# Optimization experiments

Hardware: AMD Instinct MI355X
Metric: run time of the kernel (lower is better)

The kernel has to match this reference:

```python
import jax, jax.numpy as jnp
import numpy as np

RESOLUTION = 2048
NUM_BEAMS = 256
K0 = 50.0
TWO_PI = 2.0 * np.pi


def setup_inputs() -> dict:
    key = jax.random.key(0)
    ks = jax.random.split(key, 6)
    # meshgrid buffers (indexing='ij')
    x = jnp.linspace(-1.0, 1.0, RESOLUTION, dtype=jnp.float32)
    y = jnp.linspace(-1.0, 1.0, RESOLUTION, dtype=jnp.float32)
    X, Y = jnp.meshgrid(x, y, indexing='ij')
    return {
        'theta': jax.random.uniform(ks[0], (NUM_BEAMS,), jnp.float32) * TWO_PI,
        'real': jax.random.normal(ks[1], (NUM_BEAMS,), jnp.float32) * 0.1,
        'imag': jax.random.normal(ks[2], (NUM_BEAMS,), jnp.float32) * 0.1,
        'x0': jax.random.uniform(ks[3], (NUM_BEAMS,), jnp.float32) * 2.0 - 1.0,
        'y0': jax.random.uniform(ks[4], (NUM_BEAMS,), jnp.float32) * 2.0 - 1.0,
        'log_sigma': jnp.zeros((NUM_BEAMS,), jnp.float32),
        'X': X,
        'Y': Y,
    }


def reference(theta, real, imag, x0, y0, log_sigma, X, Y):
    # Accumulate E = sum_i coeff_i * exp(i*phase_i) * envelope_i over beams,
    # carrying (E_re, E_im) through a scan so only grid-sized buffers live at once.
    def body(carry, p):
        E_re, E_im = carry
        th, re, im, px, py, ls = p
        kx = K0 * jnp.cos(th)
        ky = K0 * jnp.sin(th)
        sigma = jnp.exp(ls) + 0.001
        env = jnp.exp(-((X - px) ** 2 + (Y - py) ** 2) / sigma ** 2)
        phase = kx * X + ky * Y
        c = jnp.cos(phase)
        s = jnp.sin(phase)
        # (re + i*im) * (c + i*s) * env
        E_re = E_re + env * (re * c - im * s)
        E_im = E_im + env * (re * s + im * c)
        return (E_re, E_im), None

    params = jnp.stack([theta, real, imag, x0, y0, log_sigma], axis=1)  # [B, 6]
    zero = jnp.zeros_like(X)
    (E_re, E_im), _ = jax.lax.scan(body, (zero, zero), params)
    return E_re ** 2 + E_im ** 2  # |E|^2
```

## Files before the change

### kernel.cpp

```cpp
#include <hip/hip_runtime.h>
#include <math.h>

#define RES 2048
#define NB  256
#define PLANE (RES * NB)
#define STEP (2.0f / 2047.0f)

typedef _Float16 f16;
typedef _Float16 f16x8 __attribute__((ext_vector_type(8)));
typedef float    f32x16 __attribute__((ext_vector_type(16)));

__device__ __forceinline__ f16x8 neg8(f16x8 v) {
    union { f16x8 h; unsigned int u[4]; } x;
    x.h = v;
    #pragma unroll
    for (int i = 0; i < 4; ++i) x.u[i] ^= 0x80008000u;
    return x.h;
}


__global__ __launch_bounds__(256) void tables_frag(
    const float* __restrict__ theta, const float* __restrict__ reA,
    const float* __restrict__ imA, const float* __restrict__ x0A,
    const float* __restrict__ y0A, const float* __restrict__ lsA,
    f16* __restrict__ ws)
{
    f16* aRe = ws;
    f16* aIm = ws + PLANE;
    f16* bRe = ws + 2 * PLANE;
    f16* bIm = ws + 3 * PLANE;

    const int gid = blockIdx.x * 256 + threadIdx.x;
    const int l   = gid & 63;
    const int w   = gid >> 6;
    const int grow = (w >> 4) * 32 + (l & 31);
    const int b0   = (w & 15) * 16 + (l >> 5) * 8;
    const int e    = w * 512 + (l >> 5) * 256 + (l & 31) * 8;

    const float xv = -1.0f + (float)grow * STEP;

    float aRv[8], aIv[8], bRv[8], bIv[8];
    #pragma unroll
    for (int j = 0; j < 8; ++j) {
        const int b = b0 + j;
        const float th  = theta[b];
        const float sth = __sinf(th), cth = __cosf(th);
        const float kx = 50.0f * cth, ky = 50.0f * sth;
        const float sig = __expf(lsA[b]) + 0.001f;
        const float is2 = 1.0f / (sig * sig);
        const float re = reA[b], im = imA[b];

        const float phx = kx * xv;
        const float snx = __sinf(phx), csx = __cosf(phx);
        const float dx = xv - x0A[b];
        const float ex = __expf(-dx * dx * is2);
        aRv[j] = ex * (re * csx - im * snx);
        aIv[j] = ex * (re * snx + im * csx);

        const float phy = ky * xv;
        const float sny = __sinf(phy), csy = __cosf(phy);
        const float dy = xv - y0A[b];
        const float ey = __expf(-dy * dy * is2);
        bRv[j] = ey * csy;
        bIv[j] = ey * sny;
    }

    union { f16 h[8]; float4 v; } p;
    #pragma unroll
    for (int j = 0; j < 8; ++j) p.h[j] = (f16)aRv[j];
    *(float4*)&aRe[e] = p.v;
    #pragma unroll
    for (int j = 0; j < 8; ++j) p.h[j] = (f16)aIv[j];
    *(float4*)&aIm[e] = p.v;
    #pragma unroll
    for (int j = 0; j < 8; ++j) p.h[j] = (f16)bRv[j];
    *(float4*)&bRe[e] = p.v;
    #pragma unroll
    for (int j = 0; j < 8; ++j) p.h[j] = (f16)bIv[j];
    *(float4*)&bIm[e] = p.v;
}

__global__ __launch_bounds__(512) void gemm_frag(
    const f16* __restrict__ ws, float* __restrict__ out)
{
    const f16* aRe = ws;
    const f16* aIm = ws + PLANE;
    const f16* bRe = ws + 2 * PLANE;
    const f16* bIm = ws + 3 * PLANE;

    const int t    = threadIdx.x;
    const int lane = t & 63;
    const int wave = t >> 6;
    const int wm   = wave >> 2;
    const int wn   = wave & 3;
    const int la   = lane & 31;
    const int lg   = lane >> 5;

    const int flat = blockIdx.x;
    const int swz  = (flat & 7) * 32 + (flat >> 3);
    const int m0   = (swz >> 4) * 128;
    const int n0   = (swz & 15) * 128;

    const int laneOff = lg * 256 + la * 8;
    const int cA0 = ((m0 >> 5) + wm * 2 + 0) * 16;
    const int cA1 = ((m0 >> 5) + wm * 2 + 1) * 16;
    const int cB  = ((n0 >> 5) + wn) * 16;

    const f16* pAR0 = aRe + cA0 * 512 + laneOff;
    const f16* pAR1 = aRe + cA1 * 512 + laneOff;
    const f16* pAI0 = aIm + cA0 * 512 + laneOff;
    const f16* pAI1 = aIm + cA1 * 512 + laneOff;
    const f16* pBR  = bRe + cB  * 512 + laneOff;
    const f16* pBI  = bIm + cB  * 512 + laneOff;

    f32x16 accRe0 = (f32x16)0.0f, accIm0 = (f32x16)0.0f;
    f32x16 accRe1 = (f32x16)0.0f, accIm1 = (f32x16)0.0f;

    f16x8 aR0 = *(const f16x8*)pAR0;
    f16x8 aR1 = *(const f16x8*)pAR1;
    f16x8 aI0 = *(const f16x8*)pAI0;
    f16x8 aI1 = *(const f16x8*)pAI1;
    f16x8 bR  = *(const f16x8*)pBR;
    f16x8 bI  = *(const f16x8*)pBI;

    for (int kt = 0; kt < 16; ++kt) {
        const int nx = ((kt + 1) & 15) * 512;
        const f16x8 nR0 = *(const f16x8*)(pAR0 + nx);
        const f16x8 nR1 = *(const f16x8*)(pAR1 + nx);
        const f16x8 nI0 = *(const f16x8*)(pAI0 + nx);
        const f16x8 nI1 = *(const f16x8*)(pAI1 + nx);
        const f16x8 nBR = *(const f16x8*)(pBR  + nx);
        const f16x8 nBI = *(const f16x8*)(pBI  + nx);

        const f16x8 bN = neg8(bI);
        __builtin_amdgcn_s_setprio(1);
        accRe0 = __builtin_amdgcn_mfma_f32_32x32x16_f16(aR0, bR, accRe0, 0, 0, 0);
        accIm0 = __builtin_amdgcn_mfma_f32_32x32x16_f16(aR0, bI, accIm0, 0, 0, 0);
        accRe1 = __builtin_amdgcn_mfma_f32_32x32x16_f16(aR1, bR, accRe1, 0, 0, 0);
        accIm1 = __builtin_amdgcn_mfma_f32_32x32x16_f16(aR1, bI, accIm1, 0, 0, 0);
        accRe0 = __builtin_amdgcn_mfma_f32_32x32x16_f16(aI0, bN, accRe0, 0, 0, 0);
        accIm0 = __builtin_amdgcn_mfma_f32_32x32x16_f16(aI0, bR, accIm0, 0, 0, 0);
        accRe1 = __builtin_amdgcn_mfma_f32_32x32x16_f16(aI1, bN, accRe1, 0, 0, 0);
        accIm1 = __builtin_amdgcn_mfma_f32_32x32x16_f16(aI1, bR, accIm1, 0, 0, 0);
        __builtin_amdgcn_s_setprio(0);

        aR0 = nR0; aR1 = nR1; aI0 = nI0; aI1 = nI1; bR = nBR; bI = nBI;
    }

    const int gn     = n0 + wn * 32 + la;
    const int gmBase = m0 + wm * 64;
    #pragma unroll
    for (int r = 0; r < 16; ++r) {
        const int row = (r & 3) + 8 * (r >> 2) + 4 * lg;
        const float er = accRe0[r], ei = accIm0[r];
        out[(size_t)(gmBase + row) * RES + gn] = er * er + ei * ei;
    }
    #pragma unroll
    for (int r = 0; r < 16; ++r) {
        const int row = (r & 3) + 8 * (r >> 2) + 4 * lg;
        const float er = accRe1[r], ei = accIm1[r];
        out[(size_t)(gmBase + 32 + row) * RES + gn] = er * er + ei * ei;
    }
}

__global__ __launch_bounds__(256) void ewald_direct(
    const float* __restrict__ theta, const float* __restrict__ reA,
    const float* __restrict__ imA, const float* __restrict__ x0A,
    const float* __restrict__ y0A, const float* __restrict__ lsA,
    const float* __restrict__ X, const float* __restrict__ Y,
    float* __restrict__ out)
{
    __shared__ float kxs[NB], kys[NB], res[NB], ims[NB], pxs[NB], pys[NB], is2s[NB];
    const int t = threadIdx.x;
    if (t < NB) {
        const float th  = theta[t];
        const float sig = __expf(lsA[t]) + 0.001f;
        kxs[t] = 50.0f * __cosf(th);
        kys[t] = 50.0f * __sinf(th);
        res[t] = reA[t]; ims[t] = imA[t];
        pxs[t] = x0A[t]; pys[t] = y0A[t];
        is2s[t] = 1.0f / (sig * sig);
    }
    __syncthreads();
    const size_t npix = (size_t)RES * RES;
    for (size_t idx = (size_t)blockIdx.x * blockDim.x + t; idx < npix;
         idx += (size_t)gridDim.x * blockDim.x) {
        const float xv = X[idx], yv = Y[idx];
        float er = 0.f, ei = 0.f;
        for (int b = 0; b < NB; ++b) {
            const float dx = xv - pxs[b], dy = yv - pys[b];
            const float env = __expf(-(dx * dx + dy * dy) * is2s[b]);
            const float ph = kxs[b] * xv + kys[b] * yv;
            float s, c;
            __sincosf(ph, &s, &c);
            er += env * (res[b] * c - ims[b] * s);
            ei += env * (res[b] * s + ims[b] * c);
        }
        out[idx] = er * er + ei * ei;
    }
}

extern "C" void kernel_launch(void* const* d_in, const int* in_sizes, int n_in,
                              void* d_out, int out_size, void* d_ws, size_t ws_size,
                              hipStream_t stream) {
    const float* theta = (const float*)d_in[0];
    const float* reA   = (const float*)d_in[1];
    const float* imA   = (const float*)d_in[2];
    const float* x0A   = (const float*)d_in[3];
    const float* y0A   = (const float*)d_in[4];
    const float* lsA   = (const float*)d_in[5];
    const float* X     = (const float*)d_in[6];
    const float* Y     = (const float*)d_in[7];
    float* out = (float*)d_out;

    const size_t need = 4 * (size_t)PLANE * sizeof(f16);

    if (ws_size >= need) {
        f16* ws = (f16*)d_ws;
        tables_frag<<<256, 256, 0, stream>>>(theta, reA, imA, x0A, y0A, lsA, ws);
        gemm_frag<<<256, 512, 0, stream>>>(ws, out);
    } else {
        ewald_direct<<<2048, 256, 0, stream>>>(theta, reA, imA, x0A, y0A, lsA,
                                               X, Y, out);
    }
}
```

Before: 22.89 us.

## Stage GEMM operands through double-buffered LDS and precompute beam params in shared memory

The GEMM kernel now copies its A/B fragment tiles from global memory into a double-buffered LDS area using direct global-to-LDS loads. Waves in a block share the A tiles there instead of each loading them from global memory. Tiles shrink to 64x128 with 4 waves and 512 blocks. The table kernel computes per-beam parameters (trig of theta, sigma) once per block into shared memory instead of recomputing them per thread. This trades redundant global loads for LDS traffic and a barrier every k-step.

New measurement: 22.07 us. 1.04x faster.

```diff
diff --git a/kernel.cpp b/kernel.cpp
--- a/kernel.cpp
+++ b/kernel.cpp
@@ -9,6 +9,13 @@
 typedef _Float16 f16;
 typedef _Float16 f16x8 __attribute__((ext_vector_type(8)));
 typedef float    f32x16 __attribute__((ext_vector_type(16)));
+
+#define AS1 __attribute__((address_space(1)))
+#define AS3 __attribute__((address_space(3)))
+
+__device__ __forceinline__ void g2l16(const void* g, void* l) {
+    __builtin_amdgcn_global_load_lds((const AS1 void*)g, (AS3 void*)l, 16, 0, 0);
+}
 
 __device__ __forceinline__ f16x8 neg8(f16x8 v) {
     union { f16x8 h; unsigned int u[4]; } x;
@@ -25,12 +32,26 @@
     const float* __restrict__ y0A, const float* __restrict__ lsA,
     f16* __restrict__ ws)
 {
+    __shared__ float4 sP0[NB];
+    __shared__ float4 sP1[NB];
+
+    const int t = threadIdx.x;
+    {
+        const int b = t;
+        const float th = theta[b];
+        const float s = __sinf(th), c = __cosf(th);
+        const float sig = __expf(lsA[b]) + 0.001f;
+        sP0[b] = make_float4(50.0f * c, 50.0f * s, x0A[b], y0A[b]);
+        sP1[b] = make_float4(reA[b], imA[b], 1.0f / (sig * sig), 0.0f);
+    }
+    __syncthreads();
+
     f16* aRe = ws;
     f16* aIm = ws + PLANE;
     f16* bRe = ws + 2 * PLANE;
     f16* bIm = ws + 3 * PLANE;
 
-    const int gid = blockIdx.x * 256 + threadIdx.x;
+    const int gid = blockIdx.x * 256 + t;
     const int l   = gid & 63;
     const int w   = gid >> 6;
     const int grow = (w >> 4) * 32 + (l & 31);
@@ -43,24 +64,20 @@
     #pragma unroll
     for (int j = 0; j < 8; ++j) {
         const int b = b0 + j;
-        const float th  = theta[b];
-        const float sth = __sinf(th), cth = __cosf(th);
-        const float kx = 50.0f * cth, ky = 50.0f * sth;
-        const float sig = __expf(lsA[b]) + 0.001f;
-        const float is2 = 1.0f / (sig * sig);
-        const float re = reA[b], im = imA[b];
-
-        const float phx = kx * xv;
+        const float4 p0 = sP0[b];
+        const float4 p1 = sP1[b];
+
+        const float phx = p0.x * xv;
         const float snx = __sinf(phx), csx = __cosf(phx);
-        const float dx = xv - x0A[b];
-        const float ex = __expf(-dx * dx * is2);
-        aRv[j] = ex * (re * csx - im * snx);
-        aIv[j] = ex * (re * snx + im * csx);
-
-        const float phy = ky * xv;
+        const float dx = xv - p0.z;
+        const float ex = __expf(-dx * dx * p1.z);
+        aRv[j] = ex * (p1.x * csx - p1.y * snx);
+        aIv[j] = ex * (p1.x * snx + p1.y * csx);
+
+        const float phy = p0.y * xv;
         const float sny = __sinf(phy), csy = __cosf(phy);
-        const float dy = xv - y0A[b];
-        const float ey = __expf(-dy * dy * is2);
+        const float dy = xv - p0.w;
+        const float ey = __expf(-dy * dy * p1.z);
         bRv[j] = ey * csy;
         bIv[j] = ey * sny;
     }
@@ -80,59 +97,71 @@
     *(float4*)&bIm[e] = p.v;
 }
 
-__global__ __launch_bounds__(512) void gemm_frag(
+__global__ __launch_bounds__(256) void gemm_lds(
     const f16* __restrict__ ws, float* __restrict__ out)
 {
-    const f16* aRe = ws;
-    const f16* aIm = ws + PLANE;
-    const f16* bRe = ws + 2 * PLANE;
-    const f16* bIm = ws + 3 * PLANE;
+    __shared__ f16 lds[2][12 * 512];
 
     const int t    = threadIdx.x;
     const int lane = t & 63;
     const int wave = t >> 6;
-    const int wm   = wave >> 2;
-    const int wn   = wave & 3;
     const int la   = lane & 31;
     const int lg   = lane >> 5;
 
     const int flat = blockIdx.x;
-    const int swz  = (flat & 7) * 32 + (flat >> 3);
-    const int m0   = (swz >> 4) * 128;
-    const int n0   = (swz & 15) * 128;
-
-    const int laneOff = lg * 256 + la * 8;
-    const int cA0 = ((m0 >> 5) + wm * 2 + 0) * 16;
-    const int cA1 = ((m0 >> 5) + wm * 2 + 1) * 16;
-    const int cB  = ((n0 >> 5) + wn) * 16;
-
-    const f16* pAR0 = aRe + cA0 * 512 + laneOff;
-    const f16* pAR1 = aRe + cA1 * 512 + laneOff;
-    const f16* pAI0 = aIm + cA0 * 512 + laneOff;
-    const f16* pAI1 = aIm + cA1 * 512 + laneOff;
-    const f16* pBR  = bRe + cB  * 512 + laneOff;
-    const f16* pBI  = bIm + cB  * 512 + laneOff;
+    const int swz  = (flat & 7) * 64 + (flat >> 3);
+    const int mb   = swz >> 4;
+    const int nb   = swz & 15;
+    const int m0   = mb * 64;
+    const int n0   = nb * 128;
+
+    const f16* gsrc[3];
+    int ldst[3];
+    #pragma unroll
+    for (int j = 0; j < 3; ++j) {
+        const int idx = wave + 4 * j;
+        int p, rb;
+        if (idx < 2)      { p = 0; rb = (m0 >> 5) + idx; }
+        else if (idx < 4) { p = 1; rb = (m0 >> 5) + (idx - 2); }
+        else if (idx < 8) { p = 2; rb = (n0 >> 5) + (idx - 4); }
+        else              { p = 3; rb = (n0 >> 5) + (idx - 8); }
+        gsrc[j] = ws + (size_t)p * PLANE + rb * 16 * 512 + lane * 8;
+        ldst[j] = idx * 512;
+    }
+
+    #define STAGE(bf, kt)                                                     \
+    do {                                                                      \
+        g2l16(gsrc[0] + (kt) * 512, &lds[bf][ldst[0]]);                       \
+        g2l16(gsrc[1] + (kt) * 512, &lds[bf][ldst[1]]);                       \
+        g2l16(gsrc[2] + (kt) * 512, &lds[bf][ldst[2]]);                       \
+    } while (0)
+
+    const int lo   = lane * 8;
+    const int oAR0 = 0 * 512 + lo, oAR1 = 1 * 512 + lo;
+    const int oAI0 = 2 * 512 + lo, oAI1 = 3 * 512 + lo;
+    const int oBR  = (4 + wave) * 512 + lo;
+    const int oBI  = (8 + wave) * 512 + lo;
 
     f32x16 accRe0 = (f32x16)0.0f, accIm0 = (f32x16)0.0f;
     f32x16 accRe1 = (f32x16)0.0f, accIm1 = (f32x16)0.0f;
 
-    f16x8 aR0 = *(const f16x8*)pAR0;
-    f16x8 aR1 = *(const f16x8*)pAR1;
-    f16x8 aI0 = *(const f16x8*)pAI0;
-    f16x8 aI1 = *(const f16x8*)pAI1;
-    f16x8 bR  = *(const f16x8*)pBR;
-    f16x8 bI  = *(const f16x8*)pBI;
+    STAGE(0, 0);
+    __syncthreads();
 
     for (int kt = 0; kt < 16; ++kt) {
-        const int nx = ((kt + 1) & 15) * 512;
-        const f16x8 nR0 = *(const f16x8*)(pAR0 + nx);
-        const f16x8 nR1 = *(const f16x8*)(pAR1 + nx);
-        const f16x8 nI0 = *(const f16x8*)(pAI0 + nx);
-        const f16x8 nI1 = *(const f16x8*)(pAI1 + nx);
-        const f16x8 nBR = *(const f16x8*)(pBR  + nx);
-        const f16x8 nBI = *(const f16x8*)(pBI  + nx);
-
-        const f16x8 bN = neg8(bI);
+        const int cur = kt & 1;
+        if (kt + 1 < 16)
+            STAGE(cur ^ 1, kt + 1);
+
+        const f16* s = lds[cur];
+        const f16x8 aR0 = *(const f16x8*)(s + oAR0);
+        const f16x8 aR1 = *(const f16x8*)(s + oAR1);
+        const f16x8 aI0 = *(const f16x8*)(s + oAI0);
+        const f16x8 aI1 = *(const f16x8*)(s + oAI1);
+        const f16x8 bR  = *(const f16x8*)(s + oBR);
+        const f16x8 bI  = *(const f16x8*)(s + oBI);
+        const f16x8 bN  = neg8(bI);
+
         __builtin_amdgcn_s_setprio(1);
         accRe0 = __builtin_amdgcn_mfma_f32_32x32x16_f16(aR0, bR, accRe0, 0, 0, 0);
         accIm0 = __builtin_amdgcn_mfma_f32_32x32x16_f16(aR0, bI, accIm0, 0, 0, 0);
@@ -144,23 +173,23 @@
         accIm1 = __builtin_amdgcn_mfma_f32_32x32x16_f16(aI1, bR, accIm1, 0, 0, 0);
         __builtin_amdgcn_s_setprio(0);
 
-        aR0 = nR0; aR1 = nR1; aI0 = nI0; aI1 = nI1; bR = nBR; bI = nBI;
-    }
-
-    const int gn     = n0 + wn * 32 + la;
-    const int gmBase = m0 + wm * 64;
+        __syncthreads();
+    }
+
+    const int gn = n0 + wave * 32 + la;
     #pragma unroll
     for (int r = 0; r < 16; ++r) {
         const int row = (r & 3) + 8 * (r >> 2) + 4 * lg;
         const float er = accRe0[r], ei = accIm0[r];
-        out[(size_t)(gmBase + row) * RES + gn] = er * er + ei * ei;
+        out[(size_t)(m0 + row) * RES + gn] = er * er + ei * ei;
     }
     #pragma unroll
     for (int r = 0; r < 16; ++r) {
         const int row = (r & 3) + 8 * (r >> 2) + 4 * lg;
         const float er = accRe1[r], ei = accIm1[r];
-        out[(size_t)(gmBase + 32 + row) * RES + gn] = er * er + ei * ei;
-    }
+        out[(size_t)(m0 + 32 + row) * RES + gn] = er * er + ei * ei;
+    }
+    #undef STAGE
 }
 
 __global__ __launch_bounds__(256) void ewald_direct(
@@ -218,7 +247,7 @@
     if (ws_size >= need) {
         f16* ws = (f16*)d_ws;
         tables_frag<<<256, 256, 0, stream>>>(theta, reA, imA, x0A, y0A, lsA, ws);
-        gemm_frag<<<256, 512, 0, stream>>>(ws, out);
+        gemm_lds<<<512, 256, 0, stream>>>(ws, out);
     } else {
         ewald_direct<<<2048, 256, 0, stream>>>(theta, reA, imA, x0A, y0A, lsA,
                                                X, Y, out);
```
